# Performance work log

Measured on AMD Instinct MI355X. Metric: run time of the kernel, lower is better.

## Reference

```python
import jax, jax.numpy as jnp
import numpy as np

DIM = 512
HEADS = 8


def setup_inputs() -> dict:
    key = jax.random.key(0)
    k1, k2, k3, k4 = jax.random.split(key, 4)
    head_dim = DIM // HEADS
    scale = head_dim ** -0.5
    x = jax.random.normal(k1, (4, 4096, DIM), dtype=jnp.float32)
    Wqkv = jax.random.normal(k2, (3 * DIM, DIM), dtype=jnp.float32) * (DIM ** -0.5)
    temperature = jnp.ones((HEADS, 1, 1), dtype=jnp.float32) * scale
    Wproj = jax.random.normal(k3, (DIM, DIM), dtype=jnp.float32) * (DIM ** -0.5)
    bproj = jnp.zeros((DIM,), dtype=jnp.float32)
    return {"x": x, "Wqkv": Wqkv, "temperature": temperature, "Wproj": Wproj, "bproj": bproj}


def reference(x, Wqkv, temperature, Wproj, bproj):
    B, N, C = x.shape
    H = temperature.shape[0]
    D = C // H
    qkv = (x @ Wqkv.T).reshape(B, N, 3, H, D).transpose(2, 0, 3, 1, 4)  # (3,B,H,N,D)
    q, k, v = qkv[0], qkv[1], qkv[2]
    q = jax.nn.relu(q)
    k = jax.nn.relu(k)
    # denom = clamp(q @ sum_n k, min=100) -> (B,H,N,1)
    ksum = k.sum(axis=2)  # (B,H,D)
    denom = jnp.clip(jnp.einsum('bhnd,bhd->bhn', q, ksum), 100.0)[..., None]
    # attn = (k^T v) * temperature -> (B,H,D,D)
    attn = jnp.einsum('bhnd,bhne->bhde', k, v) * temperature
    attn1 = jnp.einsum('bhnd,bhde->bhne', q, attn)  # (B,H,N,D)
    out = attn1 / denom
    y = out.transpose(0, 2, 1, 3).reshape(B, N, C) @ Wproj.T + bproj
    return (y, attn1)
```

## Files before the change

### kernel.cpp

```cpp
#include <hip/hip_runtime.h>
#include <cstdint>
#include <cstddef>

typedef _Float16 f16;
typedef _Float16 f16x4 __attribute__((ext_vector_type(4)));
typedef _Float16 f16x8 __attribute__((ext_vector_type(8)));
typedef float f32x4 __attribute__((ext_vector_type(4)));
typedef __fp16 h2 __attribute__((ext_vector_type(2)));

#define MFMA16(a, b, c) __builtin_amdgcn_mfma_f32_16x16x32_f16(a, b, c, 0, 0, 0)

static __device__ __forceinline__ void gld16(const void* g, void* l) {
  __builtin_amdgcn_global_load_lds(
      (const __attribute__((address_space(1))) void*)g,
      (__attribute__((address_space(3))) void*)l, 16, 0, 0);
}

static __device__ __forceinline__ h2 as_h2(uint32_t u) {
  union { uint32_t u; h2 h; } c; c.u = u; return c.h;
}

#define B_ 4
#define N_ 4096
#define C_ 512
#define H_ 8
#define D_ 64
#define BN_ROWS 16384
#define QKV_COLS 1536

__global__ __launch_bounds__(256) void k_convert(
    const float* __restrict__ x, const float* __restrict__ wqkv,
    const float* __restrict__ wproj,
    f16* __restrict__ xh, f16* __restrict__ wqkvh, f16* __restrict__ wprojh)
{
  const int NX  = (BN_ROWS * C_) / 4;
  const int NW1 = (QKV_COLS * C_) / 4;
  const int NW2 = (C_ * C_) / 4;
  const int total = NX + NW1 + NW2;
  const int stride = gridDim.x * blockDim.x;
  for (int i = blockIdx.x * blockDim.x + threadIdx.x; i < total; i += stride) {
    const float4* s; f16x4* d; int j;
    if (i < NX)              { s = (const float4*)x;     d = (f16x4*)xh;     j = i; }
    else if (i < NX + NW1)   { s = (const float4*)wqkv;  d = (f16x4*)wqkvh;  j = i - NX; }
    else                     { s = (const float4*)wproj; d = (f16x4*)wprojh; j = i - NX - NW1; }
    float4 v = s[j];
    f16x4 o; o[0] = (f16)v.x; o[1] = (f16)v.y; o[2] = (f16)v.z; o[3] = (f16)v.w;
    d[j] = o;
  }
}

__global__ __launch_bounds__(256) void k_qkv_gemm(
    const f16* __restrict__ X, const f16* __restrict__ W, f16* __restrict__ Out)
{
  __shared__ f16 As[128][64];
  __shared__ f16 Bs[128][64];
  int w = (blockIdx.x & 7) * 192 + (blockIdx.x >> 3);
  const int n0 = (w % 12) * 128;
  const int m0 = (w / 12) * 128;
  const int tid = threadIdx.x;
  const int wid = tid >> 6;
  const int lane = tid & 63;
  const int lr = lane & 15, lg = lane >> 4;
  const int sr = lane >> 3;
  const int sslot = (lane & 7) ^ sr;
  const int wr = (wid >> 1) * 64, wc = (wid & 1) * 64;
  f32x4 acc[4][4] = {};
  for (int kt = 0; kt < 512; kt += 64) {
#pragma unroll
    for (int i = 0; i < 4; ++i) {
      int chunk = wid * 4 + i;
      int row = chunk * 8 + sr;
      gld16(&X[(size_t)(m0 + row) * 512 + kt + sslot * 8], &As[chunk * 8][0]);
      gld16(&W[(size_t)(n0 + row) * 512 + kt + sslot * 8], &Bs[chunk * 8][0]);
    }
    __syncthreads();
#pragma unroll
    for (int kk = 0; kk < 2; ++kk) {
      f16x8 af[4], bf[4];
#pragma unroll
      for (int m = 0; m < 4; ++m)
        af[m] = *(const f16x8*)&As[wr + m * 16 + lr][(((kk * 4 + lg) ^ (lr & 7)) * 8)];
#pragma unroll
      for (int n = 0; n < 4; ++n)
        bf[n] = *(const f16x8*)&Bs[wc + n * 16 + lr][(((kk * 4 + lg) ^ (lr & 7)) * 8)];
#pragma unroll
      for (int m = 0; m < 4; ++m)
#pragma unroll
        for (int n = 0; n < 4; ++n)
          acc[m][n] = MFMA16(bf[n], af[m], acc[m][n]);
    }
    __syncthreads();
  }
#pragma unroll
  for (int m = 0; m < 4; ++m)
#pragma unroll
    for (int n = 0; n < 4; ++n) {
      int row = m0 + wr + m * 16 + lr;
      int col = n0 + wc + n * 16 + lg * 4;
      f16x4 o;
      bool relu = (col < 1024);
#pragma unroll
      for (int j = 0; j < 4; ++j) {
        float v = acc[m][n][j];
        if (relu) v = fmaxf(v, 0.f);
        o[j] = (f16)v;
      }
      *(f16x4*)&Out[(size_t)row * QKV_COLS + col] = o;
    }
}

__global__ __launch_bounds__(256) void k_ktv(
    const f16* __restrict__ qkv, float* __restrict__ partial, float* __restrict__ pksum)
{
  __shared__ f16 ks[32][64];
  __shared__ f16 vs[32][64];
  const int bh = blockIdx.x, sp = blockIdx.y;
  const int b = bh >> 3, h = bh & 7;
  const int tid = threadIdx.x, wid = tid >> 6, lane = tid & 63;
  const int srow = lane >> 3, scol = (lane & 7) * 8;
  const int td = (wid << 2) | (lane >> 4);
  const int te = lane & 15;
  const uint32_t SEL_LO = 0x05040100u, SEL_HI = 0x07060302u;
  const h2 ones = {(__fp16)1.0f, (__fp16)1.0f};
  float acc[4][4] = {};
  float ksacc[4] = {0.f, 0.f, 0.f, 0.f};
  const size_t rowbase = (size_t)b * N_ + sp * 256;
  for (int t = 0; t < 8; ++t) {
    int nb = t * 32 + wid * 8 + srow;
    gld16(&qkv[(rowbase + nb) * QKV_COLS + 512 + h * 64 + scol], &ks[wid * 8][0]);
    gld16(&qkv[(rowbase + nb) * QKV_COLS + 1024 + h * 64 + scol], &vs[wid * 8][0]);
    __syncthreads();
#pragma unroll 4
    for (int n = 0; n < 32; n += 2) {
      uint2 ka = *(const uint2*)&ks[n][td * 4];
      uint2 kb = *(const uint2*)&ks[n + 1][td * 4];
      uint2 va = *(const uint2*)&vs[n][te * 4];
      uint2 vb = *(const uint2*)&vs[n + 1][te * 4];
      uint32_t kp[4], vp[4];
      kp[0] = __builtin_amdgcn_perm(kb.x, ka.x, SEL_LO);
      kp[1] = __builtin_amdgcn_perm(kb.x, ka.x, SEL_HI);
      kp[2] = __builtin_amdgcn_perm(kb.y, ka.y, SEL_LO);
      kp[3] = __builtin_amdgcn_perm(kb.y, ka.y, SEL_HI);
      vp[0] = __builtin_amdgcn_perm(vb.x, va.x, SEL_LO);
      vp[1] = __builtin_amdgcn_perm(vb.x, va.x, SEL_HI);
      vp[2] = __builtin_amdgcn_perm(vb.y, va.y, SEL_LO);
      vp[3] = __builtin_amdgcn_perm(vb.y, va.y, SEL_HI);
#pragma unroll
      for (int i = 0; i < 4; ++i)
#pragma unroll
        for (int j = 0; j < 4; ++j)
          acc[i][j] = __builtin_amdgcn_fdot2(as_h2(kp[i]), as_h2(vp[j]), acc[i][j], false);
      if (te == 0) {
#pragma unroll
        for (int i = 0; i < 4; ++i)
          ksacc[i] = __builtin_amdgcn_fdot2(as_h2(kp[i]), ones, ksacc[i], false);
      }
    }
    __syncthreads();
  }
  float* pp = partial + (size_t)(bh * 16 + sp) * 4096;
#pragma unroll
  for (int i = 0; i < 4; ++i)
#pragma unroll
    for (int j = 0; j < 4; ++j)
      pp[(td * 4 + i) * 64 + te * 4 + j] = acc[i][j];
  if (te == 0) {
    float* kp2 = pksum + (bh * 16 + sp) * 64;
#pragma unroll
    for (int i = 0; i < 4; ++i) kp2[td * 4 + i] = ksacc[i];
  }
}

__global__ __launch_bounds__(256) void k_reduce(
    const float* __restrict__ partial, const float* __restrict__ pksum,
    float* __restrict__ attn_acc, float* __restrict__ ksum)
{
  const int bh = blockIdx.x, seg = blockIdx.y, tid = threadIdx.x;
  const int i = seg * 256 + tid;
  float s = 0.f;
#pragma unroll 8
  for (int sp = 0; sp < 16; ++sp) s += partial[(size_t)(bh * 16 + sp) * 4096 + i];
  attn_acc[bh * 4096 + i] = s;
  if (seg == 0 && tid < 64) {
    float t2 = 0.f;
#pragma unroll 8
    for (int sp = 0; sp < 16; ++sp) t2 += pksum[(bh * 16 + sp) * 64 + tid];
    ksum[bh * 64 + tid] = t2;
  }
}

__global__ __launch_bounds__(256, 1) void k_attn_proj(
    const f16* __restrict__ qkv, const float* __restrict__ attn_acc,
    const float* __restrict__ ksum, const float* __restrict__ temp,
    const f16* __restrict__ Wp, const float* __restrict__ bias,
    float* __restrict__ attn1_out, float* __restrict__ Y)
{
  __shared__ f16 outs[64][512];
  __shared__ union {
    struct { f16 attnT[4][64][64]; f16 qs[4][64][64]; } a;
    f16 Bs[2][256][64];
  } u;
  __shared__ float ksum_s[512];
  __shared__ float bias_s[512];
  __shared__ float denom_s[4][64];

  const int bid = blockIdx.x;
  const int b = bid >> 6, sp = bid & 63;
  const size_t gr = (size_t)b * N_ + sp * 64;
  const int tid = threadIdx.x;
  const int wid = tid >> 6, lane = tid & 63;
  const int lr = lane & 15, lg = lane >> 4;
  const int sr = lane >> 3, sslot = (lane & 7) ^ sr;

  ksum_s[tid]       = ksum[b * 512 + tid];
  ksum_s[tid + 256] = ksum[b * 512 + tid + 256];
  bias_s[tid]       = bias[tid];
  bias_s[tid + 256] = bias[tid + 256];
  __syncthreads();

#pragma unroll
  for (int bi = 0; bi < 2; ++bi) {
    const int h = bi * 4 + wid;
    const float tsc = temp[h];
#pragma unroll
    for (int rr = 0; rr < 8; ++rr)
      gld16(&qkv[(gr + rr * 8 + sr) * QKV_COLS + h * 64 + sslot * 8],
            &u.a.qs[wid][rr * 8][0]);
#pragma unroll
    for (int dc = 0; dc < 4; ++dc) {
      float vals[16];
#pragma unroll
      for (int x = 0; x < 16; ++x)
        vals[x] = attn_acc[(size_t)(b * 8 + h) * 4096 + (dc * 16 + x) * 64 + lane] * tsc;
#pragma unroll
      for (int half = 0; half < 2; ++half) {
        int slot = (dc * 2 + half) ^ (lane & 7);
        f16x8 pk;
#pragma unroll
        for (int j = 0; j < 8; ++j) pk[j] = (f16)vals[half * 8 + j];
        *(f16x8*)&u.a.attnT[wid][lane][slot * 8] = pk;
      }
    }
    asm volatile("s_waitcnt vmcnt(0)" ::: "memory");
    {
      const int r = lane;
      float dot = 0.f;
#pragma unroll
      for (int c = 0; c < 8; ++c) {
        f16x8 qv = *(const f16x8*)&u.a.qs[wid][r][((c ^ (r & 7)) * 8)];
#pragma unroll
        for (int j = 0; j < 8; ++j) dot += (float)qv[j] * ksum_s[h * 64 + c * 8 + j];
      }
      denom_s[wid][r] = fmaxf(dot, 100.f);
    }
    f16x8 af[2][4], bf[4][2];
#pragma unroll
    for (int kk = 0; kk < 2; ++kk)
#pragma unroll
      for (int m = 0; m < 4; ++m)
        af[kk][m] = *(const f16x8*)&u.a.qs[wid][m * 16 + lr][(((kk * 4 + lg) ^ (lr & 7)) * 8)];
#pragma unroll
    for (int et = 0; et < 4; ++et)
#pragma unroll
      for (int kk = 0; kk < 2; ++kk)
        bf[et][kk] = *(const f16x8*)&u.a.attnT[wid][et * 16 + lr][(((kk * 4 + lg) ^ (lr & 7)) * 8)];
    f32x4 acc1[4][4] = {};
#pragma unroll
    for (int kk = 0; kk < 2; ++kk)
#pragma unroll
      for (int m = 0; m < 4; ++m)
#pragma unroll
        for (int et = 0; et < 4; ++et)
          acc1[m][et] = MFMA16(bf[et][kk], af[kk][m], acc1[m][et]);
#pragma unroll
    for (int m = 0; m < 4; ++m) {
      const int rl = m * 16 + lr;
      const float dn = denom_s[wid][rl];
#pragma unroll
      for (int et = 0; et < 4; ++et) {
        int e = et * 16 + lg * 4;
        float4 o;
        o.x = acc1[m][et][0]; o.y = acc1[m][et][1]; o.z = acc1[m][et][2]; o.w = acc1[m][et][3];
        *(float4*)&attn1_out[((size_t)(b * 8 + h) * N_ + sp * 64 + rl) * 64 + e] = o;
        f16x4 oh;
#pragma unroll
        for (int j = 0; j < 4; ++j) oh[j] = (f16)(acc1[m][et][j] / dn);
        int c = h * 64 + e;
        *(f16x4*)((char*)&outs[0][0] + rl * 1024 +
                  (((c >> 3) ^ (rl & 7)) * 16) + (lg & 1) * 8) = oh;
      }
    }
  }
  __syncthreads();

  f32x4 accP0[4][4] = {};
  f32x4 accP1[4][4] = {};

#define STAGEP(hf_, kc_, bufi)                                                \
  do {                                                                        \
    _Pragma("unroll")                                                         \
    for (int rd = 0; rd < 8; ++rd) {                                          \
      int row = rd * 32 + wid * 8;                                            \
      gld16(&Wp[(size_t)((hf_) * 256 + row + sr) * 512 + (kc_) * 64 + sslot * 8], \
            &u.Bs[bufi][row][0]);                                             \
    }                                                                         \
  } while (0)

  STAGEP(0, 0, 0);
  __syncthreads();

  for (int kc = 0; kc < 8; ++kc) {
    STAGEP(1, kc, 1);
    f16x8 afp[2][4];
#pragma unroll
    for (int kk = 0; kk < 2; ++kk)
#pragma unroll
      for (int m = 0; m < 4; ++m) {
        int row = m * 16 + lr;
        afp[kk][m] = *(const f16x8*)((const char*)&outs[0][0] + row * 1024 +
                      (((kc * 8 + kk * 4 + lg) ^ (row & 7)) * 16));
      }
    {
      f16x8 bfp[4];
#pragma unroll
      for (int kk = 0; kk < 2; ++kk) {
#pragma unroll
        for (int n = 0; n < 4; ++n)
          bfp[n] = *(const f16x8*)&u.Bs[0][wid * 64 + n * 16 + lr][(((kk * 4 + lg) ^ (lr & 7)) * 8)];
#pragma unroll
        for (int m = 0; m < 4; ++m)
#pragma unroll
          for (int n = 0; n < 4; ++n)
            accP0[m][n] = MFMA16(bfp[n], afp[kk][m], accP0[m][n]);
      }
    }
    __syncthreads();
    if (kc < 7) STAGEP(0, kc + 1, 0);
    {
      f16x8 bfp[4];
#pragma unroll
      for (int kk = 0; kk < 2; ++kk) {
#pragma unroll
        for (int n = 0; n < 4; ++n)
          bfp[n] = *(const f16x8*)&u.Bs[1][wid * 64 + n * 16 + lr][(((kk * 4 + lg) ^ (lr & 7)) * 8)];
#pragma unroll
        for (int m = 0; m < 4; ++m)
#pragma unroll
          for (int n = 0; n < 4; ++n)
            accP1[m][n] = MFMA16(bfp[n], afp[kk][m], accP1[m][n]);
      }
    }
    __syncthreads();
  }
#undef STAGEP

#pragma unroll
  for (int m = 0; m < 4; ++m)
#pragma unroll
    for (int n = 0; n < 4; ++n) {
      size_t row = gr + m * 16 + lr;
      int col0 = wid * 64 + n * 16 + lg * 4;
      float4 o0;
      o0.x = accP0[m][n][0] + bias_s[col0 + 0];
      o0.y = accP0[m][n][1] + bias_s[col0 + 1];
      o0.z = accP0[m][n][2] + bias_s[col0 + 2];
      o0.w = accP0[m][n][3] + bias_s[col0 + 3];
      *(float4*)&Y[row * C_ + col0] = o0;
      int col1 = col0 + 256;
      float4 o1;
      o1.x = accP1[m][n][0] + bias_s[col1 + 0];
      o1.y = accP1[m][n][1] + bias_s[col1 + 1];
      o1.z = accP1[m][n][2] + bias_s[col1 + 2];
      o1.w = accP1[m][n][3] + bias_s[col1 + 3];
      *(float4*)&Y[row * C_ + col1] = o1;
    }
}

extern "C" void kernel_launch(void* const* d_in, const int* in_sizes, int n_in,
                              void* d_out, int out_size, void* d_ws, size_t ws_size,
                              hipStream_t stream)
{
  const float* x     = (const float*)d_in[0];
  const float* wqkv  = (const float*)d_in[1];
  const float* temp  = (const float*)d_in[2];
  const float* wproj = (const float*)d_in[3];
  const float* bproj = (const float*)d_in[4];
  float* y_out     = (float*)d_out;
  float* attn1_out = (float*)d_out + 8388608;

  char* ws = (char*)d_ws;
  f16*   xh       = (f16*)(ws);
  float* partial  = (float*)(ws);
  f16*   wqkvh    = (f16*)(ws + 16777216);
  f16*   wprojh   = (f16*)(ws + 18350080);
  f16*   qkvh     = (f16*)(ws + 18874368);
  float* attn_acc = (float*)(ws + 69206016);
  float* ksum     = (float*)(ws + 69730304);
  float* pksum    = (float*)(ws + 69738496);

  hipLaunchKernelGGL(k_convert,   dim3(2048),   dim3(256), 0, stream, x, wqkv, wproj, xh, wqkvh, wprojh);
  hipLaunchKernelGGL(k_qkv_gemm,  dim3(1536),   dim3(256), 0, stream, xh, wqkvh, qkvh);
  hipLaunchKernelGGL(k_ktv,       dim3(32, 16), dim3(256), 0, stream, qkvh, partial, pksum);
  hipLaunchKernelGGL(k_reduce,    dim3(32, 16), dim3(256), 0, stream, partial, pksum, attn_acc, ksum);
  hipLaunchKernelGGL(k_attn_proj, dim3(256),    dim3(256), 0, stream,
                     qkvh, attn_acc, ksum, temp, wprojh, bproj, attn1_out, y_out);
}
```

Measured before the change: 111.4 us.

## Use 512 threads in attn_proj with one wave per head

The fused attention+projection kernel now launches 512 threads (8 waves), so each wave handles one head in the attention phase instead of looping over two heads. In the projection GEMM each wave owns 64 output columns instead of two 256-column halves. The q tile is staged in the per-head output buffer and the projection loop drops its double-buffered weight staging for a single buffer. This doubles wave-level parallelism per block and halves accumulator registers, at the cost of losing load/compute overlap in the projection loop and adding more barriers.

```diff
diff --git a/kernel.cpp b/kernel.cpp
--- a/kernel.cpp
+++ b/kernel.cpp
@@ -189,20 +189,20 @@
   }
 }
 
-__global__ __launch_bounds__(256, 1) void k_attn_proj(
+__global__ __launch_bounds__(512, 1) void k_attn_proj(
     const f16* __restrict__ qkv, const float* __restrict__ attn_acc,
     const float* __restrict__ ksum, const float* __restrict__ temp,
     const f16* __restrict__ Wp, const float* __restrict__ bias,
     float* __restrict__ attn1_out, float* __restrict__ Y)
 {
-  __shared__ f16 outs[64][512];
+  __shared__ f16 outs[8][64][64];
   __shared__ union {
-    struct { f16 attnT[4][64][64]; f16 qs[4][64][64]; } a;
-    f16 Bs[2][256][64];
+    f16 attnT[8][64][64];
+    f16 Bs[512][64];
   } u;
   __shared__ float ksum_s[512];
   __shared__ float bias_s[512];
-  __shared__ float denom_s[4][64];
+  __shared__ float denom_s[8][64];
 
   const int bid = blockIdx.x;
   const int b = bid >> 6, sp = bid & 63;
@@ -212,20 +212,17 @@
   const int lr = lane & 15, lg = lane >> 4;
   const int sr = lane >> 3, sslot = (lane & 7) ^ sr;
 
-  ksum_s[tid]       = ksum[b * 512 + tid];
-  ksum_s[tid + 256] = ksum[b * 512 + tid + 256];
-  bias_s[tid]       = bias[tid];
-  bias_s[tid + 256] = bias[tid + 256];
+  ksum_s[tid] = ksum[b * 512 + tid];
+  bias_s[tid] = bias[tid];
   __syncthreads();
 
-#pragma unroll
-  for (int bi = 0; bi < 2; ++bi) {
-    const int h = bi * 4 + wid;
+  {
+    const int h = wid;
     const float tsc = temp[h];
 #pragma unroll
     for (int rr = 0; rr < 8; ++rr)
       gld16(&qkv[(gr + rr * 8 + sr) * QKV_COLS + h * 64 + sslot * 8],
-            &u.a.qs[wid][rr * 8][0]);
+            &outs[h][rr * 8][0]);
 #pragma unroll
     for (int dc = 0; dc < 4; ++dc) {
       float vals[16];
@@ -238,7 +235,7 @@
         f16x8 pk;
 #pragma unroll
         for (int j = 0; j < 8; ++j) pk[j] = (f16)vals[half * 8 + j];
-        *(f16x8*)&u.a.attnT[wid][lane][slot * 8] = pk;
+        *(f16x8*)&u.attnT[h][lane][slot * 8] = pk;
       }
     }
     asm volatile("s_waitcnt vmcnt(0)" ::: "memory");
@@ -247,23 +244,23 @@
       float dot = 0.f;
 #pragma unroll
       for (int c = 0; c < 8; ++c) {
-        f16x8 qv = *(const f16x8*)&u.a.qs[wid][r][((c ^ (r & 7)) * 8)];
+        f16x8 qv = *(const f16x8*)&outs[h][r][((c ^ (r & 7)) * 8)];
 #pragma unroll
         for (int j = 0; j < 8; ++j) dot += (float)qv[j] * ksum_s[h * 64 + c * 8 + j];
       }
-      denom_s[wid][r] = fmaxf(dot, 100.f);
+      denom_s[h][r] = fmaxf(dot, 100.f);
     }
     f16x8 af[2][4], bf[4][2];
 #pragma unroll
     for (int kk = 0; kk < 2; ++kk)
 #pragma unroll
       for (int m = 0; m < 4; ++m)
-        af[kk][m] = *(const f16x8*)&u.a.qs[wid][m * 16 + lr][(((kk * 4 + lg) ^ (lr & 7)) * 8)];
+        af[kk][m] = *(const f16x8*)&outs[h][m * 16 + lr][(((kk * 4 + lg) ^ (lr & 7)) * 8)];
 #pragma unroll
     for (int et = 0; et < 4; ++et)
 #pragma unroll
       for (int kk = 0; kk < 2; ++kk)
-        bf[et][kk] = *(const f16x8*)&u.a.attnT[wid][et * 16 + lr][(((kk * 4 + lg) ^ (lr & 7)) * 8)];
+        bf[et][kk] = *(const f16x8*)&u.attnT[h][et * 16 + lr][(((kk * 4 + lg) ^ (lr & 7)) * 8)];
     f32x4 acc1[4][4] = {};
 #pragma unroll
     for (int kk = 0; kk < 2; ++kk)
@@ -275,7 +272,7 @@
 #pragma unroll
     for (int m = 0; m < 4; ++m) {
       const int rl = m * 16 + lr;
-      const float dn = denom_s[wid][rl];
+      const float dn = denom_s[h][rl];
 #pragma unroll
       for (int et = 0; et < 4; ++et) {
         int e = et * 16 + lg * 4;
@@ -285,94 +282,52 @@
         f16x4 oh;
 #pragma unroll
         for (int j = 0; j < 4; ++j) oh[j] = (f16)(acc1[m][et][j] / dn);
-        int c = h * 64 + e;
-        *(f16x4*)((char*)&outs[0][0] + rl * 1024 +
-                  (((c >> 3) ^ (rl & 7)) * 16) + (lg & 1) * 8) = oh;
+        *(f16x4*)((char*)&outs[h][rl][0] + (((e >> 3) ^ (rl & 7)) * 16) + (lg & 1) * 8) = oh;
       }
     }
   }
   __syncthreads();
 
-  f32x4 accP0[4][4] = {};
-  f32x4 accP1[4][4] = {};
-
-#define STAGEP(hf_, kc_, bufi)                                                \
-  do {                                                                        \
-    _Pragma("unroll")                                                         \
-    for (int rd = 0; rd < 8; ++rd) {                                          \
-      int row = rd * 32 + wid * 8;                                            \
-      gld16(&Wp[(size_t)((hf_) * 256 + row + sr) * 512 + (kc_) * 64 + sslot * 8], \
-            &u.Bs[bufi][row][0]);                                             \
-    }                                                                         \
-  } while (0)
-
-  STAGEP(0, 0, 0);
-  __syncthreads();
-
+  f32x4 accP[4][4] = {};
   for (int kc = 0; kc < 8; ++kc) {
-    STAGEP(1, kc, 1);
+#pragma unroll
+    for (int rd = 0; rd < 8; ++rd)
+      gld16(&Wp[(size_t)(wid * 64 + rd * 8 + sr) * 512 + kc * 64 + sslot * 8],
+            &u.Bs[wid * 64 + rd * 8][0]);
+    __syncthreads();
     f16x8 afp[2][4];
 #pragma unroll
     for (int kk = 0; kk < 2; ++kk)
 #pragma unroll
-      for (int m = 0; m < 4; ++m) {
-        int row = m * 16 + lr;
-        afp[kk][m] = *(const f16x8*)((const char*)&outs[0][0] + row * 1024 +
-                      (((kc * 8 + kk * 4 + lg) ^ (row & 7)) * 16));
-      }
-    {
+      for (int m = 0; m < 4; ++m)
+        afp[kk][m] = *(const f16x8*)&outs[kc][m * 16 + lr][(((kk * 4 + lg) ^ (lr & 7)) * 8)];
+#pragma unroll
+    for (int kk = 0; kk < 2; ++kk) {
       f16x8 bfp[4];
 #pragma unroll
-      for (int kk = 0; kk < 2; ++kk) {
+      for (int n = 0; n < 4; ++n)
+        bfp[n] = *(const f16x8*)&u.Bs[wid * 64 + n * 16 + lr][(((kk * 4 + lg) ^ (lr & 7)) * 8)];
+#pragma unroll
+      for (int m = 0; m < 4; ++m)
 #pragma unroll
         for (int n = 0; n < 4; ++n)
-          bfp[n] = *(const f16x8*)&u.Bs[0][wid * 64 + n * 16 + lr][(((kk * 4 + lg) ^ (lr & 7)) * 8)];
-#pragma unroll
-        for (int m = 0; m < 4; ++m)
-#pragma unroll
-          for (int n = 0; n < 4; ++n)
-            accP0[m][n] = MFMA16(bfp[n], afp[kk][m], accP0[m][n]);
-      }
-    }
-    __syncthreads();
-    if (kc < 7) STAGEP(0, kc + 1, 0);
-    {
-      f16x8 bfp[4];
-#pragma unroll
-      for (int kk = 0; kk < 2; ++kk) {
-#pragma unroll
-        for (int n = 0; n < 4; ++n)
-          bfp[n] = *(const f16x8*)&u.Bs[1][wid * 64 + n * 16 + lr][(((kk * 4 + lg) ^ (lr & 7)) * 8)];
-#pragma unroll
-        for (int m = 0; m < 4; ++m)
-#pragma unroll
-          for (int n = 0; n < 4; ++n)
-            accP1[m][n] = MFMA16(bfp[n], afp[kk][m], accP1[m][n]);
-      }
-    }
-    __syncthreads();
-  }
-#undef STAGEP
+          accP[m][n] = MFMA16(bfp[n], afp[kk][m], accP[m][n]);
+    }
+    __syncthreads();
+  }
 
 #pragma unroll
   for (int m = 0; m < 4; ++m)
 #pragma unroll
     for (int n = 0; n < 4; ++n) {
       size_t row = gr + m * 16 + lr;
-      int col0 = wid * 64 + n * 16 + lg * 4;
-      float4 o0;
-      o0.x = accP0[m][n][0] + bias_s[col0 + 0];
-      o0.y = accP0[m][n][1] + bias_s[col0 + 1];
-      o0.z = accP0[m][n][2] + bias_s[col0 + 2];
-      o0.w = accP0[m][n][3] + bias_s[col0 + 3];
-      *(float4*)&Y[row * C_ + col0] = o0;
-      int col1 = col0 + 256;
-      float4 o1;
-      o1.x = accP1[m][n][0] + bias_s[col1 + 0];
-      o1.y = accP1[m][n][1] + bias_s[col1 + 1];
-      o1.z = accP1[m][n][2] + bias_s[col1 + 2];
-      o1.w = accP1[m][n][3] + bias_s[col1 + 3];
-      *(float4*)&Y[row * C_ + col1] = o1;
+      int col = wid * 64 + n * 16 + lg * 4;
+      float4 o;
+      o.x = accP[m][n][0] + bias_s[col + 0];
+      o.y = accP[m][n][1] + bias_s[col + 1];
+      o.z = accP[m][n][2] + bias_s[col + 2];
+      o.w = accP[m][n][3] + bias_s[col + 3];
+      *(float4*)&Y[row * C_ + col] = o;
     }
 }
 
@@ -402,6 +357,6 @@
   hipLaunchKernelGGL(k_qkv_gemm,  dim3(1536),   dim3(256), 0, stream, xh, wqkvh, qkvh);
   hipLaunchKernelGGL(k_ktv,       dim3(32, 16), dim3(256), 0, stream, qkvh, partial, pksum);
   hipLaunchKernelGGL(k_reduce,    dim3(32, 16), dim3(256), 0, stream, partial, pksum, attn_acc, ksum);
-  hipLaunchKernelGGL(k_attn_proj, dim3(256),    dim3(256), 0, stream,
+  hipLaunchKernelGGL(k_attn_proj, dim3(256),    dim3(512), 0, stream,
                      qkvh, attn_acc, ksum, temp, wprojh, bproj, attn1_out, y_out);
 }
```

After: 107.4 us. -3.6%, faster.
